# Kernel optimization log

Hardware: AMD Instinct MI355X
Metric: run time of the kernel (lower is better)

Reference implementation:

```python
import jax, jax.numpy as jnp
import numpy as np

NUM_CLASSES = 1000
GAMMA = 0.9
N = 131072


def setup_inputs() -> dict:
    key = jax.random.key(0)
    k1, k2, k3 = jax.random.split(key, 3)
    preds = jax.random.normal(k1, (N, NUM_CLASSES), dtype=jnp.float32)
    labels = jax.random.randint(k2, (N,), 0, NUM_CLASSES)
    val_preds = jax.random.normal(k3, (NUM_CLASSES, NUM_CLASSES), dtype=jnp.float32)
    return {"preds": preds, "labels": labels, "val_preds": val_preds}


def reference(preds, labels, val_preds):
    # Equivalent of ValScores.update: per-class mean of preds (label-indexed
    # segment reduction) followed by an EMA update, skipping empty classes.
    C = val_preds.shape[0]
    # sums[c] = sum of preds rows with label c   -> [C, C]
    sums = jax.ops.segment_sum(preds, labels, num_segments=C)
    # counts[c] = number of rows with label c    -> [C]
    counts = jax.ops.segment_sum(jnp.ones((preds.shape[0],), preds.dtype),
                                 labels, num_segments=C)
    has = counts > 0
    means = sums / jnp.where(has, counts, jnp.ones_like(counts))[:, None]
    new_val = jnp.where(has[:, None],
                        (1.0 - GAMMA) * means + GAMMA * val_preds,
                        val_preds)
    return new_val
```

## Files before the change

kernel.cpp:

```cpp
#include <hip/hip_runtime.h>

#define NUM_C 1000
#define COLS4 250
#define GAMMA 0.9f

typedef float v4f __attribute__((ext_vector_type(4)));

__global__ void count_kernel(const int* __restrict__ labels,
                             int* __restrict__ counts, int n) {
    int i = blockIdx.x * blockDim.x + threadIdx.x;
    if (i < n) atomicAdd(&counts[labels[i]], 1);
}

__global__ void scan_kernel(const int* __restrict__ counts,
                            int* __restrict__ offsets) {
    __shared__ int s[1024];
    int tid = threadIdx.x;
    int v = (tid < NUM_C) ? counts[tid] : 0;
    s[tid] = v;
    __syncthreads();
    for (int d = 1; d < 1024; d <<= 1) {
        int x = (tid >= d) ? s[tid - d] : 0;
        __syncthreads();
        s[tid] += x;
        __syncthreads();
    }
    if (tid < NUM_C) offsets[tid] = s[tid] - v;
}

__global__ void scatter_kernel(const int* __restrict__ labels,
                               const int* __restrict__ offsets,
                               int* __restrict__ cursors,
                               int* __restrict__ rowidx, int n) {
    int i = blockIdx.x * blockDim.x + threadIdx.x;
    if (i < n) {
        int l = labels[i];
        int pos = offsets[l] + atomicAdd(&cursors[l], 1);
        rowidx[pos] = i;
    }
}

__global__ __launch_bounds__(256) void accum_kernel(
        const float* __restrict__ preds, const float* __restrict__ val,
        const int* __restrict__ counts, const int* __restrict__ offsets,
        const int* __restrict__ rowidx, float* __restrict__ out) {
    const int c   = blockIdx.x;
    const int tid = threadIdx.x;
    const bool active = (tid < COLS4);
    const int col4 = active ? tid : 0;

    const v4f* __restrict__ pv = (const v4f*)preds;
    const v4f* __restrict__ vv = (const v4f*)val;
    v4f* __restrict__ ov = (v4f*)out;
    const size_t crow = (size_t)c * COLS4;

    const int nc  = counts[c];
    const int off = offsets[c];

    if (nc == 0) {
        if (active) ov[crow + col4] = vv[crow + col4];
        return;
    }

    __shared__ int rows_s[512];
    v4f acc0 = {0.f, 0.f, 0.f, 0.f};
    v4f acc1 = {0.f, 0.f, 0.f, 0.f};

    for (int base = 0; base < nc; base += 512) {
        int m = min(nc - base, 512);
        if (tid < m) rows_s[tid] = rowidx[off + base + tid];
        if (tid + 256 < m) rows_s[tid + 256] = rowidx[off + base + tid + 256];
        __syncthreads();

        int r = 0;
        for (; r + 8 <= m; r += 8) {
            size_t i0 = (size_t)rows_s[r + 0] * COLS4 + col4;
            size_t i1 = (size_t)rows_s[r + 1] * COLS4 + col4;
            size_t i2 = (size_t)rows_s[r + 2] * COLS4 + col4;
            size_t i3 = (size_t)rows_s[r + 3] * COLS4 + col4;
            size_t i4 = (size_t)rows_s[r + 4] * COLS4 + col4;
            size_t i5 = (size_t)rows_s[r + 5] * COLS4 + col4;
            size_t i6 = (size_t)rows_s[r + 6] * COLS4 + col4;
            size_t i7 = (size_t)rows_s[r + 7] * COLS4 + col4;
            v4f v0 = __builtin_nontemporal_load(&pv[i0]);
            v4f v1 = __builtin_nontemporal_load(&pv[i1]);
            v4f v2 = __builtin_nontemporal_load(&pv[i2]);
            v4f v3 = __builtin_nontemporal_load(&pv[i3]);
            v4f v4 = __builtin_nontemporal_load(&pv[i4]);
            v4f v5 = __builtin_nontemporal_load(&pv[i5]);
            v4f v6 = __builtin_nontemporal_load(&pv[i6]);
            v4f v7 = __builtin_nontemporal_load(&pv[i7]);
            acc0 += (v0 + v1) + (v2 + v3);
            acc1 += (v4 + v5) + (v6 + v7);
        }
        for (; r < m; r++) {
            size_t i0 = (size_t)rows_s[r] * COLS4 + col4;
            acc0 += __builtin_nontemporal_load(&pv[i0]);
        }
        __syncthreads();
    }

    if (active) {
        float inv = 1.0f / (float)nc;
        v4f s = acc0 + acc1;
        v4f vp = vv[crow + col4];
        v4f o = (1.0f - GAMMA) * (s * inv) + GAMMA * vp;
        ov[crow + col4] = o;
    }
}

extern "C" void kernel_launch(void* const* d_in, const int* in_sizes, int n_in,
                              void* d_out, int out_size, void* d_ws, size_t ws_size,
                              hipStream_t stream) {
    const float* preds  = (const float*)d_in[0];
    const int*   labels = (const int*)d_in[1];
    const float* val    = (const float*)d_in[2];
    float*       out    = (float*)d_out;
    const int n = in_sizes[1];

    char* ws = (char*)d_ws;
    int* counts  = (int*)(ws + 0);
    int* offsets = (int*)(ws + 4096);
    int* cursors = (int*)(ws + 8192);
    int* rowidx  = (int*)(ws + 12288);

    (void)hipMemsetAsync(d_ws, 0, 12288, stream);
    count_kernel<<<(n + 255) / 256, 256, 0, stream>>>(labels, counts, n);
    scan_kernel<<<1, 1024, 0, stream>>>(counts, offsets);
    scatter_kernel<<<(n + 255) / 256, 256, 0, stream>>>(labels, offsets, cursors, rowidx, n);
    accum_kernel<<<NUM_C, 256, 0, stream>>>(preds, val, counts, offsets, rowidx, out);
}
```

Measured before the change: 705.9 us.

## Record atomic rank in count pass and split class rows across two half-blocks

New measurement: 710.9 us. No clear change (+0.7%).

```diff
diff --git a/kernel.cpp b/kernel.cpp
--- a/kernel.cpp
+++ b/kernel.cpp
@@ -6,10 +6,14 @@
 
 typedef float v4f __attribute__((ext_vector_type(4)));
 
-__global__ void count_kernel(const int* __restrict__ labels,
-                             int* __restrict__ counts, int n) {
+__global__ void count_rank_kernel(const int* __restrict__ labels,
+                                  int* __restrict__ counts,
+                                  int* __restrict__ rank, int n) {
     int i = blockIdx.x * blockDim.x + threadIdx.x;
-    if (i < n) atomicAdd(&counts[labels[i]], 1);
+    if (i < n) {
+        int l = labels[i];
+        rank[i] = atomicAdd(&counts[l], 1);
+    }
 }
 
 __global__ void scan_kernel(const int* __restrict__ counts,
@@ -30,24 +34,24 @@
 
 __global__ void scatter_kernel(const int* __restrict__ labels,
                                const int* __restrict__ offsets,
-                               int* __restrict__ cursors,
+                               const int* __restrict__ rank,
                                int* __restrict__ rowidx, int n) {
     int i = blockIdx.x * blockDim.x + threadIdx.x;
     if (i < n) {
-        int l = labels[i];
-        int pos = offsets[l] + atomicAdd(&cursors[l], 1);
-        rowidx[pos] = i;
+        rowidx[offsets[labels[i]] + rank[i]] = i;
     }
 }
 
-__global__ __launch_bounds__(256) void accum_kernel(
+__global__ __launch_bounds__(512) void accum_kernel(
         const float* __restrict__ preds, const float* __restrict__ val,
         const int* __restrict__ counts, const int* __restrict__ offsets,
         const int* __restrict__ rowidx, float* __restrict__ out) {
-    const int c   = blockIdx.x;
-    const int tid = threadIdx.x;
-    const bool active = (tid < COLS4);
-    const int col4 = active ? tid : 0;
+    const int c    = blockIdx.x;
+    const int tid  = threadIdx.x;
+    const int half = tid >> 8;
+    const int lane = tid & 255;
+    const bool active = (lane < COLS4);
+    const int col4 = active ? lane : 0;
 
     const v4f* __restrict__ pv = (const v4f*)preds;
     const v4f* __restrict__ vv = (const v4f*)val;
@@ -58,51 +62,47 @@
     const int off = offsets[c];
 
     if (nc == 0) {
-        if (active) ov[crow + col4] = vv[crow + col4];
+        if (half == 0 && active) ov[crow + col4] = vv[crow + col4];
         return;
     }
 
     __shared__ int rows_s[512];
+    __shared__ v4f red[COLS4];
+
     v4f acc0 = {0.f, 0.f, 0.f, 0.f};
     v4f acc1 = {0.f, 0.f, 0.f, 0.f};
 
     for (int base = 0; base < nc; base += 512) {
         int m = min(nc - base, 512);
         if (tid < m) rows_s[tid] = rowidx[off + base + tid];
-        if (tid + 256 < m) rows_s[tid + 256] = rowidx[off + base + tid + 256];
         __syncthreads();
 
-        int r = 0;
-        for (; r + 8 <= m; r += 8) {
+        int r = half;
+        for (; r + 6 < m; r += 8) {
             size_t i0 = (size_t)rows_s[r + 0] * COLS4 + col4;
-            size_t i1 = (size_t)rows_s[r + 1] * COLS4 + col4;
-            size_t i2 = (size_t)rows_s[r + 2] * COLS4 + col4;
-            size_t i3 = (size_t)rows_s[r + 3] * COLS4 + col4;
-            size_t i4 = (size_t)rows_s[r + 4] * COLS4 + col4;
-            size_t i5 = (size_t)rows_s[r + 5] * COLS4 + col4;
-            size_t i6 = (size_t)rows_s[r + 6] * COLS4 + col4;
-            size_t i7 = (size_t)rows_s[r + 7] * COLS4 + col4;
-            v4f v0 = __builtin_nontemporal_load(&pv[i0]);
-            v4f v1 = __builtin_nontemporal_load(&pv[i1]);
-            v4f v2 = __builtin_nontemporal_load(&pv[i2]);
-            v4f v3 = __builtin_nontemporal_load(&pv[i3]);
-            v4f v4 = __builtin_nontemporal_load(&pv[i4]);
-            v4f v5 = __builtin_nontemporal_load(&pv[i5]);
-            v4f v6 = __builtin_nontemporal_load(&pv[i6]);
-            v4f v7 = __builtin_nontemporal_load(&pv[i7]);
-            acc0 += (v0 + v1) + (v2 + v3);
-            acc1 += (v4 + v5) + (v6 + v7);
+            size_t i1 = (size_t)rows_s[r + 2] * COLS4 + col4;
+            size_t i2 = (size_t)rows_s[r + 4] * COLS4 + col4;
+            size_t i3 = (size_t)rows_s[r + 6] * COLS4 + col4;
+            v4f v0 = pv[i0];
+            v4f v1 = pv[i1];
+            v4f v2 = pv[i2];
+            v4f v3 = pv[i3];
+            acc0 += v0 + v1;
+            acc1 += v2 + v3;
         }
-        for (; r < m; r++) {
+        for (; r < m; r += 2) {
             size_t i0 = (size_t)rows_s[r] * COLS4 + col4;
-            acc0 += __builtin_nontemporal_load(&pv[i0]);
+            acc0 += pv[i0];
         }
         __syncthreads();
     }
 
-    if (active) {
+    v4f acc = acc0 + acc1;
+    if (half == 1 && active) red[col4] = acc;
+    __syncthreads();
+    if (half == 0 && active) {
         float inv = 1.0f / (float)nc;
-        v4f s = acc0 + acc1;
+        v4f s = acc + red[col4];
         v4f vp = vv[crow + col4];
         v4f o = (1.0f - GAMMA) * (s * inv) + GAMMA * vp;
         ov[crow + col4] = o;
@@ -121,12 +121,12 @@
     char* ws = (char*)d_ws;
     int* counts  = (int*)(ws + 0);
     int* offsets = (int*)(ws + 4096);
-    int* cursors = (int*)(ws + 8192);
-    int* rowidx  = (int*)(ws + 12288);
+    int* rank    = (int*)(ws + 8192);
+    int* rowidx  = (int*)(ws + 8192 + (size_t)n * 4);
 
-    (void)hipMemsetAsync(d_ws, 0, 12288, stream);
-    count_kernel<<<(n + 255) / 256, 256, 0, stream>>>(labels, counts, n);
+    (void)hipMemsetAsync(d_ws, 0, 4096, stream);
+    count_rank_kernel<<<(n + 255) / 256, 256, 0, stream>>>(labels, counts, rank, n);
     scan_kernel<<<1, 1024, 0, stream>>>(counts, offsets);
-    scatter_kernel<<<(n + 255) / 256, 256, 0, stream>>>(labels, offsets, cursors, rowidx, n);
-    accum_kernel<<<NUM_C, 256, 0, stream>>>(preds, val, counts, offsets, rowidx, out);
+    scatter_kernel<<<(n + 255) / 256, 256, 0, stream>>>(labels, offsets, rank, rowidx, n);
+    accum_kernel<<<NUM_C, 512, 0, stream>>>(preds, val, counts, offsets, rowidx, out);
 }
```
